# Optimization experiments

Measured on AMD Instinct MI355X. Metric: run time of the kernel, lower is better.

Reference implementation:

```python
import jax, jax.numpy as jnp
import numpy as np

H = 8          # n_heads
D_HEAD = 64    # head_dim; scores scaled by sqrt(D_HEAD)


def setup_inputs() -> dict:
    key = jax.random.key(0)
    ks = jax.random.split(key, 9)
    B, S, Dm = 8, 1024, 512
    return {
        "input_Q": jax.random.normal(ks[0], (B, S, Dm), jnp.float32),
        "input_K": jax.random.normal(ks[1], (B, S, Dm), jnp.float32),
        "input_V": jax.random.normal(ks[2], (B, S, Dm), jnp.float32),
        "attn_mask": jax.random.randint(ks[3], (B, S, S), 0, 2).astype(bool),
        "edge_encoding": jax.random.normal(ks[4], (B, S, S), jnp.float32),
        "W_Q": jax.random.normal(ks[5], (Dm, Dm), jnp.float32) / np.sqrt(Dm),
        "W_K": jax.random.normal(ks[6], (Dm, Dm), jnp.float32) / np.sqrt(Dm),
        "W_V": jax.random.normal(ks[7], (Dm, Dm), jnp.float32) / np.sqrt(Dm),
        "W_fc": jax.random.normal(ks[8], (Dm, Dm), jnp.float32) / np.sqrt(Dm),
    }


def reference(input_Q, input_K, input_V, attn_mask, edge_encoding, W_Q, W_K, W_V, W_fc):
    B, S, Dm = input_Q.shape
    # project and split heads: [B, H, S, d_head]
    def heads(x, W):
        return (x @ W).reshape(B, S, H, D_HEAD).transpose(0, 2, 1, 3)
    Q = heads(input_Q, W_Q)
    K = heads(input_K, W_K)
    V = heads(input_V, W_V)
    scores = jnp.einsum("bhqd,bhkd->bhqk", Q, K) / np.sqrt(D_HEAD)
    scores = scores + edge_encoding[:, None, :, :]
    scores = jnp.where(attn_mask[:, None, :, :], jnp.float32(-1e9), scores)
    attn = jax.nn.softmax(scores, axis=-1)
    context = jnp.einsum("bhqk,bhkd->bhqd", attn, V)
    context = context.transpose(0, 2, 1, 3).reshape(B, S, Dm)
    output = context @ W_fc
    scores_avg = scores.sum(axis=1) / H  # [B, S, S]
    return output, scores_avg
```

## Files before the change

kernel.cpp:

```cpp
#include <hip/hip_runtime.h>
#include <math.h>

#define B_ 8
#define S_ 1024
#define DM 512
#define H_ 8
#define DH 64

typedef _Float16 h4 __attribute__((ext_vector_type(4)));
typedef _Float16 h8 __attribute__((ext_vector_type(8)));
typedef float f4 __attribute__((ext_vector_type(4)));

#define MFMA16(a, b, c) __builtin_amdgcn_mfma_f32_16x16x32_f16(a, b, c, 0, 0, 0)

__global__ __launch_bounds__(256) void cast_x(
    const float* __restrict__ x0, const float* __restrict__ x1,
    const float* __restrict__ x2, _Float16* __restrict__ y0,
    _Float16* __restrict__ y1, _Float16* __restrict__ y2) {
  const float* x = (blockIdx.y == 0) ? x0 : (blockIdx.y == 1) ? x1 : x2;
  _Float16* y = (blockIdx.y == 0) ? y0 : (blockIdx.y == 1) ? y1 : y2;
  size_t i = (size_t)blockIdx.x * 1024 + (size_t)threadIdx.x * 4;
  float4 v = *(const float4*)(x + i);
  h4 hv = {(_Float16)v.x, (_Float16)v.y, (_Float16)v.z, (_Float16)v.w};
  *(h4*)(y + i) = hv;
}

__global__ __launch_bounds__(256) void cast_w(
    const float* __restrict__ w0, const float* __restrict__ w1,
    const float* __restrict__ w2, const float* __restrict__ w3,
    _Float16* __restrict__ t0, _Float16* __restrict__ t1,
    _Float16* __restrict__ t2, _Float16* __restrict__ t3) {
  const float* W;
  _Float16* T;
  switch (blockIdx.z) {
    case 0: W = w0; T = t0; break;
    case 1: W = w1; T = t1; break;
    case 2: W = w2; T = t2; break;
    default: W = w3; T = t3; break;
  }
  __shared__ _Float16 ts[64][72];
  const int t = threadIdx.x;
  const int r = t >> 2, c0 = (t & 3) * 16;
  const int n0 = blockIdx.x * 64, k0 = blockIdx.y * 64;
#pragma unroll
  for (int i = 0; i < 4; i++) {
    float4 v = *(const float4*)&W[(size_t)(k0 + r) * 512 + n0 + c0 + i * 4];
    h4 hv = {(_Float16)v.x, (_Float16)v.y, (_Float16)v.z, (_Float16)v.w};
    *(h4*)&ts[r][c0 + i * 4] = hv;
  }
  __syncthreads();
  alignas(16) _Float16 outv[16];
#pragma unroll
  for (int i = 0; i < 16; i++) outv[i] = ts[c0 + i][r];
  *(uint4*)&T[(size_t)(n0 + r) * 512 + k0 + c0] = *(uint4*)&outv[0];
  *(uint4*)&T[(size_t)(n0 + r) * 512 + k0 + c0 + 8] = *(uint4*)&outv[8];
}

__global__ __launch_bounds__(256) void gemm_qkv(
    const _Float16* __restrict__ Xq, const _Float16* __restrict__ Xk,
    const _Float16* __restrict__ Xv, const _Float16* __restrict__ Wt,
    _Float16* __restrict__ Qh, _Float16* __restrict__ Kh,
    _Float16* __restrict__ Vth) {
  const int z = blockIdx.z;
  const int id = blockIdx.x + 4 * blockIdx.y;
  const int c = id & 7, r = id >> 3;
  const int by = c + 8 * (r & 7);
  const int bx = r >> 3;
  const _Float16* A = (z == 0) ? Xq : (z == 1) ? Xk : Xv;
  const _Float16* Bt = Wt + (size_t)z * 512 * 512;
  __shared__ _Float16 Sh[128 * 144];
  const int t = threadIdx.x, lane = t & 63, w = t >> 6;
  const int quad = lane >> 4, l16 = lane & 15;
  const int row0 = by * 128, col0 = bx * 128;
  const int wm = (w & 1) * 64, wn = (w >> 1) * 64;
  f4 acc[4][4] = {};
  const _Float16* Ab = A + (size_t)(row0 + wm + l16) * DM + quad * 8;
  const _Float16* Bb = Bt + (size_t)(col0 + wn + l16) * DM + quad * 8;
  for (int k0 = 0; k0 < DM; k0 += 64) {
    h8 af[4][2], bf[4][2];
#pragma unroll
    for (int m = 0; m < 4; m++) {
      const _Float16* ap = Ab + (size_t)m * 16 * DM + k0;
      const _Float16* bp = Bb + (size_t)m * 16 * DM + k0;
      af[m][0] = *(const h8*)ap;
      af[m][1] = *(const h8*)(ap + 32);
      bf[m][0] = *(const h8*)bp;
      bf[m][1] = *(const h8*)(bp + 32);
    }
#pragma unroll
    for (int m = 0; m < 4; m++)
#pragma unroll
      for (int n = 0; n < 4; n++) {
        acc[m][n] = MFMA16(af[m][0], bf[n][0], acc[m][n]);
        acc[m][n] = MFMA16(af[m][1], bf[n][1], acc[m][n]);
      }
  }
  if (z < 2) {
    _Float16* C = (z == 0) ? Qh : Kh;
#pragma unroll
    for (int m = 0; m < 4; m++)
#pragma unroll
      for (int n = 0; n < 4; n++)
#pragma unroll
        for (int reg = 0; reg < 4; reg++)
          Sh[(wm + m * 16 + quad * 4 + reg) * 144 + wn + n * 16 + l16] =
              (_Float16)acc[m][n][reg];
    __syncthreads();
    const int rr = t >> 4;
    const int cs = (t & 15) * 8;
#pragma unroll
    for (int i = 0; i < 8; i++) {
      int row = rr + 16 * i;
      *(uint4*)&C[(size_t)(row0 + row) * DM + col0 + cs] =
          *(uint4*)&Sh[row * 144 + cs];
    }
  } else {
#pragma unroll
    for (int m = 0; m < 4; m++)
#pragma unroll
      for (int n = 0; n < 4; n++) {
        h4 vv = {(_Float16)acc[m][n][0], (_Float16)acc[m][n][1],
                 (_Float16)acc[m][n][2], (_Float16)acc[m][n][3]};
        *(h4*)&Sh[(wn + n * 16 + l16) * 144 + wm + m * 16 + quad * 4] = vv;
      }
    __syncthreads();
    const int rr = t >> 4;
    const int cs = (t & 15) * 8;
    const int b = row0 >> 10, s0 = row0 & 1023;
#pragma unroll
    for (int i = 0; i < 8; i++) {
      int cg = col0 + rr + 16 * i;
      int h = cg >> 6, d = cg & 63;
      *(uint4*)&Vth[((size_t)(b * 8 + h) * 64 + d) * S_ + s0 + cs] =
          *(uint4*)&Sh[(rr + 16 * i) * 144 + cs];
    }
  }
}

__global__ __launch_bounds__(256) void gemm_fc(
    const _Float16* __restrict__ A, const _Float16* __restrict__ Bt,
    float* __restrict__ C) {
  const int id = blockIdx.x + 4 * blockIdx.y;
  const int c = id & 7, r = id >> 3;
  const int by = c + 8 * (r & 15);
  const int bx = r >> 4;
  const int t = threadIdx.x, lane = t & 63, w = t >> 6;
  const int quad = lane >> 4, l16 = lane & 15;
  const int row0 = by * 64, col0 = bx * 128;
  const int wm = (w & 1) * 32, wn = (w >> 1) * 64;
  f4 acc[2][4] = {};
  const _Float16* Ab = A + (size_t)(row0 + wm + l16) * DM + quad * 8;
  const _Float16* Bb = Bt + (size_t)(col0 + wn + l16) * DM + quad * 8;
  for (int k0 = 0; k0 < DM; k0 += 64) {
    h8 af[2][2], bf[4][2];
#pragma unroll
    for (int m = 0; m < 2; m++) {
      const _Float16* ap = Ab + (size_t)m * 16 * DM + k0;
      af[m][0] = *(const h8*)ap;
      af[m][1] = *(const h8*)(ap + 32);
    }
#pragma unroll
    for (int n = 0; n < 4; n++) {
      const _Float16* bp = Bb + (size_t)n * 16 * DM + k0;
      bf[n][0] = *(const h8*)bp;
      bf[n][1] = *(const h8*)(bp + 32);
    }
#pragma unroll
    for (int m = 0; m < 2; m++)
#pragma unroll
      for (int n = 0; n < 4; n++) {
        acc[m][n] = MFMA16(af[m][0], bf[n][0], acc[m][n]);
        acc[m][n] = MFMA16(af[m][1], bf[n][1], acc[m][n]);
      }
  }
#pragma unroll
  for (int m = 0; m < 2; m++)
#pragma unroll
    for (int n = 0; n < 4; n++)
#pragma unroll
      for (int reg = 0; reg < 4; reg++) {
        size_t row = row0 + wm + m * 16 + quad * 4 + reg;
        size_t col = col0 + wn + n * 16 + l16;
        C[row * DM + col] = acc[m][n][reg];
      }
}

__global__ __launch_bounds__(256) void scores_mfma(
    const _Float16* __restrict__ Qh, const _Float16* __restrict__ Kh,
    const int* __restrict__ mask, const float* __restrict__ edge,
    float* __restrict__ out1, _Float16* __restrict__ Ehs) {
  const int b = blockIdx.z;
  const int id = blockIdx.x + 8 * blockIdx.y;
  const int iy = id & 7, jx = id >> 3;
  const int i0 = iy * 128, j0 = jx * 128;
  const _Float16* A = Qh + (size_t)b * S_ * DM;
  const _Float16* Bt = Kh + (size_t)b * S_ * DM;
  const int t = threadIdx.x, lane = t & 63, w = t >> 6;
  const int quad = lane >> 4, l16 = lane & 15;
  const int wm = (w & 1) * 64, wn = (w >> 1) * 64;
  f4 acc[4][4] = {};
  const _Float16* Ab = A + (size_t)(i0 + wm + l16) * DM + quad * 8;
  const _Float16* Bb = Bt + (size_t)(j0 + wn + l16) * DM + quad * 8;
  for (int k0 = 0; k0 < DM; k0 += 64) {
    h8 af[4][2], bf[4][2];
#pragma unroll
    for (int m = 0; m < 4; m++) {
      const _Float16* ap = Ab + (size_t)m * 16 * DM + k0;
      const _Float16* bp = Bb + (size_t)m * 16 * DM + k0;
      af[m][0] = *(const h8*)ap;
      af[m][1] = *(const h8*)(ap + 32);
      bf[m][0] = *(const h8*)bp;
      bf[m][1] = *(const h8*)(bp + 32);
    }
#pragma unroll
    for (int m = 0; m < 4; m++)
#pragma unroll
      for (int n = 0; n < 4; n++) {
        acc[m][n] = MFMA16(af[m][0], bf[n][0], acc[m][n]);
        acc[m][n] = MFMA16(af[m][1], bf[n][1], acc[m][n]);
      }
  }
  const int jt_base = j0 >> 6;
#pragma unroll
  for (int m = 0; m < 4; m++)
#pragma unroll
    for (int reg = 0; reg < 4; reg++) {
      size_t gi = i0 + wm + m * 16 + quad * 4 + reg;
      size_t rowb = ((size_t)b * S_ + gi) * S_;
      const int jt = jt_base + (wn >> 6);
      size_t ehrow = (((size_t)b * 16 + jt) * 1024 + gi) * 64 + l16 * 4;
      h4 ev;
#pragma unroll
      for (int n = 0; n < 4; n++) {
        size_t idx = rowb + j0 + wn + n * 16 + l16;
        int mk = mask[idx];
        float e = edge[idx];
        out1[idx] = mk ? -1e9f : (acc[m][n][reg] * (1.0f / 64.0f) + e);
        ev[n] = mk ? (_Float16)(-65504.0f) : (_Float16)e;
      }
      *(h4*)&Ehs[ehrow] = ev;
    }
}

__global__ __launch_bounds__(256) void flash_mfma(
    const _Float16* __restrict__ Qh, const _Float16* __restrict__ Kh,
    const _Float16* __restrict__ Vth, const _Float16* __restrict__ Ehs,
    _Float16* __restrict__ ctxh) {
  __shared__ _Float16 Ps[128][72];
  const int t = threadIdx.x, lane = t & 63, w = t >> 6;
  const int quad = lane >> 4, l16 = lane & 15;
  const int g = blockIdx.x + 8 * blockIdx.y;
  const int c = g & 7, r = g >> 3;
  const int bh = c + 8 * (r & 7);
  const int qb = r >> 3;
  const int b = bh >> 3, h = bh & 7;
  const int q0 = qb * 128;
  const size_t bS = (size_t)b * S_;
  const int qw = w * 32;

  h8 aq[2][2];
#pragma unroll
  for (int m = 0; m < 2; m++)
#pragma unroll
    for (int k = 0; k < 2; k++)
      aq[m][k] = *(const h8*)&Qh[(bS + q0 + qw + m * 16 + l16) * DM + h * DH +
                                 k * 32 + quad * 8];

  f4 acco[2][4] = {};
  float m_run[2][4], l_run[2][4];
#pragma unroll
  for (int m = 0; m < 2; m++)
#pragma unroll
    for (int rr = 0; rr < 4; rr++) {
      m_run[m][rr] = -INFINITY;
      l_run[m][rr] = 0.f;
    }

  const _Float16* Kb = Kh + bS * DM + h * DH + quad * 8;
  const _Float16* Vb = Vth + (size_t)bh * 64 * S_ + quad * 8;

  for (int kb = 0; kb < S_; kb += 64) {
    const size_t ehb = ((size_t)b * 16 + (kb >> 6)) * 1024;
    h4 evh[2][4];
#pragma unroll
    for (int m = 0; m < 2; m++)
#pragma unroll
      for (int reg = 0; reg < 4; reg++)
        evh[m][reg] =
            *(const h4*)&Ehs[(ehb + q0 + qw + m * 16 + quad * 4 + reg) * 64 +
                             l16 * 4];
    f4 accs[2][4] = {};
#pragma unroll
    for (int n = 0; n < 4; n++) {
      const _Float16* kp = Kb + (size_t)(kb + n * 16 + l16) * DM;
      h8 b0 = *(const h8*)kp;
      h8 b1 = *(const h8*)(kp + 32);
#pragma unroll
      for (int m = 0; m < 2; m++) {
        accs[m][n] = MFMA16(aq[m][0], b0, accs[m][n]);
        accs[m][n] = MFMA16(aq[m][1], b1, accs[m][n]);
      }
    }
    float sv[2][4][4];
#pragma unroll
    for (int m = 0; m < 2; m++)
#pragma unroll
      for (int n = 0; n < 4; n++)
#pragma unroll
        for (int reg = 0; reg < 4; reg++)
          sv[m][n][reg] = accs[m][n][reg] * 0.125f + (float)evh[m][reg][n];
#pragma unroll
    for (int m = 0; m < 2; m++)
#pragma unroll
      for (int reg = 0; reg < 4; reg++) {
        float mx = fmaxf(fmaxf(sv[m][0][reg], sv[m][1][reg]),
                         fmaxf(sv[m][2][reg], sv[m][3][reg]));
#pragma unroll
        for (int off = 1; off < 16; off <<= 1)
          mx = fmaxf(mx, __shfl_xor(mx, off, 16));
        float mnew = fmaxf(m_run[m][reg], mx);
        float alpha = __expf(m_run[m][reg] - mnew);
        m_run[m][reg] = mnew;
        float psum = 0.f;
#pragma unroll
        for (int n = 0; n < 4; n++) {
          float p = __expf(sv[m][n][reg] - mnew);
          sv[m][n][reg] = p;
          psum += p;
        }
#pragma unroll
        for (int off = 1; off < 16; off <<= 1)
          psum += __shfl_xor(psum, off, 16);
        l_run[m][reg] = l_run[m][reg] * alpha + psum;
#pragma unroll
        for (int d = 0; d < 4; d++) acco[m][d][reg] *= alpha;
      }
#pragma unroll
    for (int m = 0; m < 2; m++)
#pragma unroll
      for (int n = 0; n < 4; n++)
#pragma unroll
        for (int reg = 0; reg < 4; reg++)
          Ps[qw + m * 16 + quad * 4 + reg][n * 16 + l16] =
              (_Float16)sv[m][n][reg];
    h8 ap[2][2];
#pragma unroll
    for (int m = 0; m < 2; m++)
#pragma unroll
      for (int k = 0; k < 2; k++)
        ap[m][k] = *(h8*)&Ps[qw + m * 16 + l16][k * 32 + quad * 8];
#pragma unroll
    for (int d = 0; d < 4; d++) {
      const _Float16* vp = Vb + (size_t)(d * 16 + l16) * S_ + kb;
      h8 bv0 = *(const h8*)vp;
      h8 bv1 = *(const h8*)(vp + 32);
#pragma unroll
      for (int m = 0; m < 2; m++) {
        acco[m][d] = MFMA16(ap[m][0], bv0, acco[m][d]);
        acco[m][d] = MFMA16(ap[m][1], bv1, acco[m][d]);
      }
    }
  }
#pragma unroll
  for (int m = 0; m < 2; m++)
#pragma unroll
    for (int d = 0; d < 4; d++)
#pragma unroll
      for (int reg = 0; reg < 4; reg++)
        Ps[qw + m * 16 + quad * 4 + reg][d * 16 + l16] =
            (_Float16)(acco[m][d][reg] / l_run[m][reg]);
  __syncthreads();
  const int orr = t >> 3, ocs = (t & 7) * 8;
#pragma unroll
  for (int i = 0; i < 4; i++) {
    int row = orr + 32 * i;
    *(uint4*)&ctxh[(bS + q0 + row) * DM + h * DH + ocs] =
        *(uint4*)&Ps[row][ocs];
  }
}

extern "C" void kernel_launch(void* const* d_in, const int* in_sizes, int n_in,
                              void* d_out, int out_size, void* d_ws,
                              size_t ws_size, hipStream_t stream) {
  const float* Xq = (const float*)d_in[0];
  const float* Xk = (const float*)d_in[1];
  const float* Xv = (const float*)d_in[2];
  const int* mask = (const int*)d_in[3];
  const float* edge = (const float*)d_in[4];
  const float* Wq = (const float*)d_in[5];
  const float* Wk = (const float*)d_in[6];
  const float* Wv = (const float*)d_in[7];
  const float* Wfc = (const float*)d_in[8];

  float* out0 = (float*)d_out;
  float* out1 = out0 + (size_t)B_ * S_ * DM;

  const size_t NE = (size_t)B_ * S_ * DM;
  char* ws = (char*)d_ws;
  _Float16* Qh = (_Float16*)ws;
  _Float16* Kh = Qh + NE;
  _Float16* Vth = Kh + NE;
  _Float16* Xhq = Vth + NE;
  _Float16* Xhk = Xhq + NE;
  _Float16* Xhv = Xhk + NE;
  _Float16* Wt = Xhv + NE;
  _Float16* Wtf = Wt + 3 * 512 * 512;
  _Float16* Ehs = Wt + 4 * 512 * 512;
  _Float16* ctxh = Xhq;

  dim3 blk(256);
  cast_x<<<dim3(4096, 3), blk, 0, stream>>>(Xq, Xk, Xv, Xhq, Xhk, Xhv);
  cast_w<<<dim3(8, 8, 4), blk, 0, stream>>>(Wq, Wk, Wv, Wfc, Wt,
                                            Wt + 512 * 512, Wt + 2 * 512 * 512,
                                            Wtf);
  gemm_qkv<<<dim3(4, 64, 3), blk, 0, stream>>>(Xhq, Xhk, Xhv, Wt, Qh, Kh, Vth);
  scores_mfma<<<dim3(8, 8, 8), blk, 0, stream>>>(Qh, Kh, mask, edge, out1,
                                                 Ehs);
  flash_mfma<<<dim3(8, 64), blk, 0, stream>>>(Qh, Kh, Vth, Ehs, ctxh);
  gemm_fc<<<dim3(4, 128), blk, 0, stream>>>(ctxh, Wtf, out0);
}
```

Before: 408.2 us.

## Stage K/V tiles through LDS with register prefetch in flash attention kernel

The flash attention kernel now cooperatively loads each 64-key K and V^T tile into shared memory once per block instead of having each of the four waves read them from global memory. The next tile's K, V and edge-bias values are prefetched into registers while the current tile is computed, overlapping global latency with the MFMA work. Q is also loaded coalesced through LDS. This cuts redundant global/L2 traffic across waves, at the cost of two barriers per iteration, higher register pressure and extra LDS use that may reduce occupancy.

```diff
diff --git a/kernel.cpp b/kernel.cpp
--- a/kernel.cpp
+++ b/kernel.cpp
@@ -246,7 +246,7 @@
     const _Float16* __restrict__ Qh, const _Float16* __restrict__ Kh,
     const _Float16* __restrict__ Vth, const _Float16* __restrict__ Ehs,
     _Float16* __restrict__ ctxh) {
-  __shared__ _Float16 Ps[128][72];
+  __shared__ _Float16 Ps[128][72], Ks[64][72], Vt[64][72];
   const int t = threadIdx.x, lane = t & 63, w = t >> 6;
   const int quad = lane >> 4, l16 = lane & 15;
   const int g = blockIdx.x + 8 * blockIdx.y;
@@ -256,15 +256,35 @@
   const int b = bh >> 3, h = bh & 7;
   const int q0 = qb * 128;
   const size_t bS = (size_t)b * S_;
+  const int sr = t >> 3, sc = (t & 7) * 8;
   const int qw = w * 32;
 
+#pragma unroll
+  for (int i = 0; i < 4; i++)
+    *(uint4*)&Ps[sr + 32 * i][sc] =
+        *(const uint4*)&Qh[(bS + q0 + sr + 32 * i) * DM + h * DH + sc];
+  __syncthreads();
   h8 aq[2][2];
 #pragma unroll
   for (int m = 0; m < 2; m++)
 #pragma unroll
     for (int k = 0; k < 2; k++)
-      aq[m][k] = *(const h8*)&Qh[(bS + q0 + qw + m * 16 + l16) * DM + h * DH +
-                                 k * 32 + quad * 8];
+      aq[m][k] = *(h8*)&Ps[qw + m * 16 + l16][k * 32 + quad * 8];
+
+  uint4 kv[4];
+  kv[0] = *(const uint4*)&Kh[(bS + sr) * DM + h * DH + sc];
+  kv[1] = *(const uint4*)&Kh[(bS + sr + 32) * DM + h * DH + sc];
+  kv[2] = *(const uint4*)&Vth[((size_t)bh * 64 + sr) * S_ + sc];
+  kv[3] = *(const uint4*)&Vth[((size_t)bh * 64 + sr + 32) * S_ + sc];
+  h4 evh[2][4];
+#pragma unroll
+  for (int m = 0; m < 2; m++)
+#pragma unroll
+    for (int reg = 0; reg < 4; reg++)
+      evh[m][reg] = *(const h4*)&Ehs[(((size_t)b * 16 + 0) * 1024 + q0 + qw +
+                                      m * 16 + quad * 4 + reg) *
+                                         64 +
+                                     l16 * 4];
 
   f4 acco[2][4] = {};
   float m_run[2][4], l_run[2][4];
@@ -276,25 +296,34 @@
       l_run[m][rr] = 0.f;
     }
 
-  const _Float16* Kb = Kh + bS * DM + h * DH + quad * 8;
-  const _Float16* Vb = Vth + (size_t)bh * 64 * S_ + quad * 8;
-
   for (int kb = 0; kb < S_; kb += 64) {
-    const size_t ehb = ((size_t)b * 16 + (kb >> 6)) * 1024;
-    h4 evh[2][4];
-#pragma unroll
-    for (int m = 0; m < 2; m++)
-#pragma unroll
-      for (int reg = 0; reg < 4; reg++)
-        evh[m][reg] =
-            *(const h4*)&Ehs[(ehb + q0 + qw + m * 16 + quad * 4 + reg) * 64 +
-                             l16 * 4];
+    __syncthreads();
+    *(uint4*)&Ks[sr][sc] = kv[0];
+    *(uint4*)&Ks[sr + 32][sc] = kv[1];
+    *(uint4*)&Vt[sr][sc] = kv[2];
+    *(uint4*)&Vt[sr + 32][sc] = kv[3];
+    __syncthreads();
+    const int kn = kb + 64;
+    h4 evn[2][4];
+    if (kn < S_) {
+      kv[0] = *(const uint4*)&Kh[(bS + kn + sr) * DM + h * DH + sc];
+      kv[1] = *(const uint4*)&Kh[(bS + kn + sr + 32) * DM + h * DH + sc];
+      kv[2] = *(const uint4*)&Vth[((size_t)bh * 64 + sr) * S_ + kn + sc];
+      kv[3] = *(const uint4*)&Vth[((size_t)bh * 64 + sr + 32) * S_ + kn + sc];
+      const size_t ehb = ((size_t)b * 16 + (kn >> 6)) * 1024;
+#pragma unroll
+      for (int m = 0; m < 2; m++)
+#pragma unroll
+        for (int reg = 0; reg < 4; reg++)
+          evn[m][reg] =
+              *(const h4*)&Ehs[(ehb + q0 + qw + m * 16 + quad * 4 + reg) * 64 +
+                               l16 * 4];
+    }
     f4 accs[2][4] = {};
 #pragma unroll
     for (int n = 0; n < 4; n++) {
-      const _Float16* kp = Kb + (size_t)(kb + n * 16 + l16) * DM;
-      h8 b0 = *(const h8*)kp;
-      h8 b1 = *(const h8*)(kp + 32);
+      h8 b0 = *(h8*)&Ks[n * 16 + l16][quad * 8];
+      h8 b1 = *(h8*)&Ks[n * 16 + l16][32 + quad * 8];
 #pragma unroll
       for (int m = 0; m < 2; m++) {
         accs[m][n] = MFMA16(aq[m][0], b0, accs[m][n]);
@@ -351,14 +380,19 @@
         ap[m][k] = *(h8*)&Ps[qw + m * 16 + l16][k * 32 + quad * 8];
 #pragma unroll
     for (int d = 0; d < 4; d++) {
-      const _Float16* vp = Vb + (size_t)(d * 16 + l16) * S_ + kb;
-      h8 bv0 = *(const h8*)vp;
-      h8 bv1 = *(const h8*)(vp + 32);
+      h8 bv0 = *(h8*)&Vt[d * 16 + l16][quad * 8];
+      h8 bv1 = *(h8*)&Vt[d * 16 + l16][32 + quad * 8];
 #pragma unroll
       for (int m = 0; m < 2; m++) {
         acco[m][d] = MFMA16(ap[m][0], bv0, acco[m][d]);
         acco[m][d] = MFMA16(ap[m][1], bv1, acco[m][d]);
       }
+    }
+    if (kn < S_) {
+#pragma unroll
+      for (int m = 0; m < 2; m++)
+#pragma unroll
+        for (int reg = 0; reg < 4; reg++) evh[m][reg] = evn[m][reg];
     }
   }
 #pragma unroll
```

Result: faster. 356.0 us (-12.8%).
